# Kernel optimization log

Hardware: AMD Instinct MI355X
Metric: run time of the kernel (lower is better)

## Reference

```python
import jax, jax.numpy as jnp
import numpy as np

N = 50000      # nodes
E = 800000     # edges
F_IN = 11      # node feature dim (from docstring)
HID = 128      # hidden_channels
NC = 16        # num_classes
G = 64         # number of graphs in the batch
NEG_SLOPE = 0.2


def gat_layer(h_in, src, dst, W, a_src, a_dst, b, n_nodes):
    """Single-head GATConv with self-loops (PyG defaults, edge_attr unused)."""
    h = h_in @ W                                   # [N, C]
    alpha_s = h @ a_src                            # [N]
    alpha_d = h @ a_dst                            # [N]
    e = jax.nn.leaky_relu(alpha_s[src] + alpha_d[dst], NEG_SLOPE)  # [E']
    # segment softmax over incoming edges of each dst node
    m = jax.ops.segment_max(e, dst, num_segments=n_nodes)
    ex = jnp.exp(e - m[dst])
    den = jax.ops.segment_sum(ex, dst, num_segments=n_nodes)
    alpha = ex / den[dst]                          # [E']
    out = jax.ops.segment_sum(alpha[:, None] * h[src], dst, num_segments=n_nodes)
    return out + b


def setup_inputs() -> dict:
    key = jax.random.key(0)
    ks = jax.random.split(key, 16)
    glorot = lambda k, fi, fo: jax.random.normal(k, (fi, fo), jnp.float32) * np.float32(1.0 / np.sqrt(fi))
    inp = {
        "x": jax.random.normal(ks[0], (N, F_IN), jnp.float32),
        "edge_index": jax.random.randint(ks[1], (2, E), 0, N, dtype=jnp.int32),
        "edge_attr": jax.random.normal(ks[2], (E, 17), jnp.float32),
        "batch": jnp.sort(jax.random.randint(ks[3], (N,), 0, G, dtype=jnp.int32)),
        "W1": glorot(ks[4], F_IN, HID), "as1": jax.random.normal(ks[5], (HID,)) * 0.1,
        "ad1": jax.random.normal(ks[6], (HID,)) * 0.1, "b1": jnp.zeros((HID,), jnp.float32),
        "W2": glorot(ks[7], HID, HID), "as2": jax.random.normal(ks[8], (HID,)) * 0.1,
        "ad2": jax.random.normal(ks[9], (HID,)) * 0.1, "b2": jnp.zeros((HID,), jnp.float32),
        "W3": glorot(ks[10], HID, NC), "as3": jax.random.normal(ks[11], (NC,)) * 0.1,
        "ad3": jax.random.normal(ks[12], (NC,)) * 0.1, "b3": jnp.zeros((NC,), jnp.float32),
    }
    return inp


def reference(x, edge_index, edge_attr, batch,
              W1, as1, ad1, b1, W2, as2, ad2, b2, W3, as3, ad3, b3):
    n = x.shape[0]
    loop = jnp.arange(n, dtype=edge_index.dtype)
    src = jnp.concatenate([edge_index[0], loop])   # add self-loops
    dst = jnp.concatenate([edge_index[1], loop])

    h = jax.nn.relu(gat_layer(x, src, dst, W1, as1, ad1, b1, n))
    h = jax.nn.relu(gat_layer(h, src, dst, W2, as2, ad2, b2, n))
    h = jax.nn.relu(gat_layer(h, src, dst, W3, as3, ad3, b3, n))

    # global mean pool over graphs
    sums = jax.ops.segment_sum(h, batch, num_segments=G)              # [G, NC]
    cnts = jax.ops.segment_sum(jnp.ones((n,), h.dtype), batch, num_segments=G)
    pooled = sums / jnp.maximum(cnts, 1.0)[:, None]
    # dropout is identity in eval mode
    return jax.nn.sigmoid(pooled)
```

## Files before the change

kernel.cpp:

```cpp
#include <hip/hip_runtime.h>
#include <hip/hip_bf16.h>
#include <hip/hip_fp16.h>
#include <math.h>

#define N_NODES 50000
#define N_EDGES 800000
#define F_IN    11
#define HID     128
#define NC      16
#define NG      64
#define E_TOT   (N_EDGES + N_NODES)
#define NBLK_POOL ((N_NODES + 255) / 256)
#define NEG_SLOPE 0.2f

#define NB   ((N_NODES + 63) >> 6)
#define BCAP 4096
#define NHB  ((N_EDGES + 4095) / 4096)

typedef _Float16 half_t;
typedef __attribute__((ext_vector_type(2))) _Float16 half2v;
typedef __attribute__((ext_vector_type(4))) _Float16 half4;
typedef __attribute__((ext_vector_type(8))) _Float16 half8;
typedef __attribute__((ext_vector_type(4))) float f32x4;

__device__ __forceinline__ float leaky(float x) { return x >= 0.f ? x : NEG_SLOPE * x; }


__global__ __launch_bounds__(256) void bucket_hist_w2t_kernel(const int* __restrict__ ei,
                                                              int* __restrict__ gcount,
                                                              const float* __restrict__ W2,
                                                              half_t* __restrict__ W2T) {
    int tid = threadIdx.x;
    if (blockIdx.x >= NHB) {
        int id = (blockIdx.x - NHB) * 256 + tid;
        if (id < HID * HID) {
            int col = id >> 7, k = id & 127;
            W2T[id] = (half_t)W2[k * HID + col];
        }
        return;
    }
    __shared__ int cnt[NB];
    for (int i = tid; i < NB; i += 256) cnt[i] = 0;
    __syncthreads();
    int e0 = blockIdx.x * 4096 + tid;
#pragma unroll
    for (int k = 0; k < 16; ++k) {
        int e = e0 + k * 256;
        if (e < N_EDGES) atomicAdd(&cnt[ei[N_EDGES + e] >> 6], 1);
    }
    __syncthreads();
    for (int i = tid; i < NB; i += 256)
        if (cnt[i]) atomicAdd(&gcount[i], cnt[i]);
}

__global__ void scanB_kernel(const int* __restrict__ gcount, int* __restrict__ bOff,
                             int* __restrict__ gcur) {
    __shared__ int ls[1024];
    int tid = threadIdx.x;
    int v = 0;
    if (tid < NB) {
        int sl = N_NODES - (tid << 6);
        sl = sl > 64 ? 64 : sl;
        v = gcount[tid] + sl;
    }
    ls[tid] = v;
    __syncthreads();
    for (int ofs = 1; ofs < 1024; ofs <<= 1) {
        int x = (tid >= ofs) ? ls[tid - ofs] : 0;
        __syncthreads();
        ls[tid] += x;
        __syncthreads();
    }
    int excl = (tid > 0) ? ls[tid - 1] : 0;
    if (tid < NB) { bOff[tid] = excl; gcur[tid] = excl; }
    if (tid == 0) bOff[NB] = E_TOT;
}

__global__ __launch_bounds__(256) void bucket_scatter_kernel(const int* __restrict__ ei,
                                                             int* __restrict__ gcur,
                                                             unsigned* __restrict__ pairs) {
    __shared__ int cnt[NB];
    __shared__ int base[NB];
    int tid = threadIdx.x;
    for (int i = tid; i < NB; i += 256) cnt[i] = 0;
    __syncthreads();
    int s[16], d[16];
    int e0 = blockIdx.x * 4096 + tid;
#pragma unroll
    for (int k = 0; k < 16; ++k) {
        int e = e0 + k * 256;
        if (e < N_EDGES) { s[k] = ei[e]; d[k] = ei[N_EDGES + e]; }
        else if (e < E_TOT) { s[k] = d[k] = e - N_EDGES; }
        else d[k] = -1;
        if (d[k] >= 0) atomicAdd(&cnt[d[k] >> 6], 1);
    }
    __syncthreads();
    for (int i = tid; i < NB; i += 256)
        base[i] = cnt[i] ? atomicAdd(&gcur[i], cnt[i]) : 0;
    __syncthreads();
    for (int i = tid; i < NB; i += 256) cnt[i] = 0;
    __syncthreads();
#pragma unroll
    for (int k = 0; k < 16; ++k) {
        if (d[k] >= 0) {
            int b = d[k] >> 6;
            int r = atomicAdd(&cnt[b], 1);
            pairs[base[b] + r] = (unsigned)s[k] | ((unsigned)(d[k] & 63) << 16);
        }
    }
}

__global__ __launch_bounds__(256) void csr_finalize_kernel(const unsigned* __restrict__ pairs,
                                                           const int* __restrict__ bOff,
                                                           int* __restrict__ off,
                                                           int* __restrict__ csr) {
    __shared__ unsigned lp[BCAP];
    __shared__ int deg[64], offs[65], cnt[64];
    int b = blockIdx.x, tid = threadIdx.x;
    int d0 = b << 6;
    int nd = N_NODES - d0; nd = nd > 64 ? 64 : nd;
    int lo = bOff[b], hi = bOff[b + 1], n = hi - lo;
    if (tid < 64) { deg[tid] = 0; cnt[tid] = 0; }
    __syncthreads();
    bool staged = (n <= BCAP);
    for (int i = tid; i < n; i += 256) {
        unsigned p = pairs[lo + i];
        if (staged) lp[i] = p;
        atomicAdd(&deg[p >> 16], 1);
    }
    __syncthreads();
    if (tid == 0) {
        int a = 0;
#pragma unroll
        for (int i = 0; i < 64; ++i) { offs[i] = a; a += deg[i]; }
        offs[64] = a;
    }
    __syncthreads();
    if (tid < nd) off[d0 + tid] = lo + offs[tid];
    if (b == (int)gridDim.x - 1 && tid == 0) off[N_NODES] = E_TOT;
    for (int i = tid; i < n; i += 256) {
        unsigned p = staged ? lp[i] : pairs[lo + i];
        int ld = p >> 16;
        int r = atomicAdd(&cnt[ld], 1);
        csr[lo + offs[ld] + r] = (int)(p & 0xFFFF);
    }
}


__global__ void gemm1_kernel(const float* __restrict__ x, const float* __restrict__ W,
                             const float* __restrict__ a_s, const float* __restrict__ a_d,
                             half_t* __restrict__ h16,
                             float* __restrict__ asv, float* __restrict__ adv) {
    __shared__ float xr[F_IN];
    __shared__ float red[4];
    int row = blockIdx.x;
    int t = threadIdx.x;
    if (t < F_IN) xr[t] = x[row * F_IN + t];
    __syncthreads();
    float acc = 0.f;
#pragma unroll
    for (int k = 0; k < F_IN; ++k) acc = fmaf(xr[k], W[k * HID + t], acc);
    h16[(size_t)row * HID + t] = (half_t)acc;
    float ps = acc * a_s[t], pd = acc * a_d[t];
#pragma unroll
    for (int m = 32; m; m >>= 1) { ps += __shfl_xor(ps, m); pd += __shfl_xor(pd, m); }
    int lane = t & 63, wid = t >> 6;
    if (lane == 0) { red[wid * 2] = ps; red[wid * 2 + 1] = pd; }
    __syncthreads();
    if (t == 0) { asv[row] = red[0] + red[2]; adv[row] = red[1] + red[3]; }
}


__global__ __launch_bounds__(256) void gemm2_mfma_kernel(
    const half_t* __restrict__ A, const half_t* __restrict__ W2T,
    const float* __restrict__ a_s, const float* __restrict__ a_d,
    half_t* __restrict__ outp, float* __restrict__ asv, float* __restrict__ adv) {
    int wid = threadIdx.x >> 6;
    int lane = threadIdx.x & 63;
    int row0 = blockIdx.x * 64 + wid * 16;
    int rl = lane & 15;
    int kg = lane >> 4;
    int arow = row0 + rl;
    if (arow >= N_NODES) arow = N_NODES - 1;
    const half8* Ap = (const half8*)(A + (size_t)arow * HID);
    half8 afrag[4];
#pragma unroll
    for (int kk = 0; kk < 4; ++kk) afrag[kk] = Ap[kk * 4 + kg];
    float ps[4] = {0.f, 0.f, 0.f, 0.f}, pd[4] = {0.f, 0.f, 0.f, 0.f};
#pragma unroll
    for (int ct = 0; ct < 8; ++ct) {
        f32x4 acc = {0.f, 0.f, 0.f, 0.f};
        const half8* Bp = (const half8*)(W2T + (size_t)(ct * 16 + rl) * HID);
#pragma unroll
        for (int kk = 0; kk < 4; ++kk)
            acc = __builtin_amdgcn_mfma_f32_16x16x32_f16(afrag[kk], Bp[kk * 4 + kg], acc, 0, 0, 0);
        int col = ct * 16 + rl;
        float as_c = a_s[col], ad_c = a_d[col];
#pragma unroll
        for (int i = 0; i < 4; ++i) {
            int r = row0 + kg * 4 + i;
            ps[i] = fmaf(acc[i], as_c, ps[i]);
            pd[i] = fmaf(acc[i], ad_c, pd[i]);
            if (r < N_NODES) outp[(size_t)r * HID + col] = (half_t)acc[i];
        }
    }
#pragma unroll
    for (int m = 1; m <= 8; m <<= 1) {
#pragma unroll
        for (int i = 0; i < 4; ++i) { ps[i] += __shfl_xor(ps[i], m); pd[i] += __shfl_xor(pd[i], m); }
    }
    if (rl == 0) {
#pragma unroll
        for (int i = 0; i < 4; ++i) {
            int r = row0 + kg * 4 + i;
            if (r < N_NODES) { asv[r] = ps[i]; adv[r] = pd[i]; }
        }
    }
}


__global__ __launch_bounds__(256) void gemm3_kernel(const half_t* __restrict__ A16,
                                                    const float* __restrict__ W,
                                                    const float* __restrict__ a_s,
                                                    const float* __restrict__ a_d,
                                                    half_t* __restrict__ outp,
                                                    float* __restrict__ asv,
                                                    float* __restrict__ adv) {
    __shared__ float hs[16][HID + 1];
    int tid = threadIdx.x;
    int row0 = blockIdx.x * 16;
    for (int i = tid; i < 16 * HID; i += 256) {
        int r = i >> 7, c = i & 127;
        int gr = row0 + r;
        hs[r][c] = (gr < N_NODES) ? (float)A16[(size_t)gr * HID + c] : 0.f;
    }
    __syncthreads();
    int col = tid & 15, r = tid >> 4;
    float acc = 0.f;
#pragma unroll 4
    for (int k = 0; k < HID; ++k) acc = fmaf(hs[r][k], W[k * NC + col], acc);
    int gr = row0 + r;
    float ps = acc * a_s[col], pd = acc * a_d[col];
#pragma unroll
    for (int m = 1; m <= 8; m <<= 1) { ps += __shfl_xor(ps, m); pd += __shfl_xor(pd, m); }
    if (gr < N_NODES) {
        outp[(size_t)gr * NC + col] = (half_t)acc;
        if (col == 0) { asv[gr] = ps; adv[gr] = pd; }
    }
}


__global__ __launch_bounds__(256) void agg128_kernel(
    const half_t* __restrict__ h16, const int* __restrict__ off, const int* __restrict__ csr,
    const float* __restrict__ asv, const float* __restrict__ adv,
    const float* __restrict__ bias, half_t* __restrict__ outp) {
    int lane = threadIdx.x & 63;
    int n = (blockIdx.x * blockDim.x + threadIdx.x) >> 6;
    if (n >= N_NODES) return;
    int o0 = off[n], o1 = off[n + 1];
    float ad_n = adv[n];
    int half = lane >> 5;
    int qc = lane & 31;
    const half4* hp = (const half4*)h16;
    float m = -INFINITY, den = 0.f;
    float4 acc = make_float4(0.f, 0.f, 0.f, 0.f);
    for (int base = o0; base < o1; base += 64) {
        int j = base + lane;
        bool valid = j < o1;
        int s = valid ? csr[j] : 0;
        float e = valid ? leaky(asv[s] + ad_n) : -INFINITY;
        float cm = e;
#pragma unroll
        for (int k = 32; k; k >>= 1) cm = fmaxf(cm, __shfl_xor(cm, k));
        float nm = fmaxf(m, cm);
        float rs = __expf(m - nm);
        den *= rs; acc.x *= rs; acc.y *= rs; acc.z *= rs; acc.w *= rs;
        float w = valid ? __expf(e - nm) : 0.f;
        float ws = w;
#pragma unroll
        for (int k = 32; k; k >>= 1) ws += __shfl_xor(ws, k);
        den += ws;
        m = nm;
        int cnt = min(64, o1 - base);
        int t = 0;
        for (; t + 16 <= cnt; t += 16) {
            int sv[8]; float wv[8]; half4 vv[8];
#pragma unroll
            for (int u = 0; u < 8; ++u) {
                sv[u] = __shfl(s, t + 2 * u + half);
                wv[u] = __shfl(w, t + 2 * u + half);
            }
#pragma unroll
            for (int u = 0; u < 8; ++u) vv[u] = hp[(size_t)sv[u] * 32 + qc];
#pragma unroll
            for (int u = 0; u < 8; ++u) {
                acc.x = fmaf(wv[u], (float)vv[u].x, acc.x);
                acc.y = fmaf(wv[u], (float)vv[u].y, acc.y);
                acc.z = fmaf(wv[u], (float)vv[u].z, acc.z);
                acc.w = fmaf(wv[u], (float)vv[u].w, acc.w);
            }
        }
        for (; t + 8 <= cnt; t += 8) {
            int sv[4]; float wv[4]; half4 vv[4];
#pragma unroll
            for (int u = 0; u < 4; ++u) {
                sv[u] = __shfl(s, t + 2 * u + half);
                wv[u] = __shfl(w, t + 2 * u + half);
            }
#pragma unroll
            for (int u = 0; u < 4; ++u) vv[u] = hp[(size_t)sv[u] * 32 + qc];
#pragma unroll
            for (int u = 0; u < 4; ++u) {
                acc.x = fmaf(wv[u], (float)vv[u].x, acc.x);
                acc.y = fmaf(wv[u], (float)vv[u].y, acc.y);
                acc.z = fmaf(wv[u], (float)vv[u].z, acc.z);
                acc.w = fmaf(wv[u], (float)vv[u].w, acc.w);
            }
        }
        for (; t + 2 <= cnt; t += 2) {
            int s0 = __shfl(s, t + half);
            float w0 = __shfl(w, t + half);
            half4 v0 = hp[(size_t)s0 * 32 + qc];
            acc.x = fmaf(w0, (float)v0.x, acc.x); acc.y = fmaf(w0, (float)v0.y, acc.y);
            acc.z = fmaf(w0, (float)v0.z, acc.z); acc.w = fmaf(w0, (float)v0.w, acc.w);
        }
        if (t < cnt) {
            int s0 = __shfl(s, t);
            float w0 = __shfl(w, t);
            if (half == 0) {
                half4 v0 = hp[(size_t)s0 * 32 + qc];
                acc.x = fmaf(w0, (float)v0.x, acc.x); acc.y = fmaf(w0, (float)v0.y, acc.y);
                acc.z = fmaf(w0, (float)v0.z, acc.z); acc.w = fmaf(w0, (float)v0.w, acc.w);
            }
        }
    }
    acc.x += __shfl_xor(acc.x, 32); acc.y += __shfl_xor(acc.y, 32);
    acc.z += __shfl_xor(acc.z, 32); acc.w += __shfl_xor(acc.w, 32);
    if (half == 0) {
        float inv = 1.f / den;
        float4 bv = ((const float4*)bias)[qc];
        half4 o;
        o.x = (half_t)fmaxf(fmaf(acc.x, inv, bv.x), 0.f);
        o.y = (half_t)fmaxf(fmaf(acc.y, inv, bv.y), 0.f);
        o.z = (half_t)fmaxf(fmaf(acc.z, inv, bv.z), 0.f);
        o.w = (half_t)fmaxf(fmaf(acc.w, inv, bv.w), 0.f);
        ((half4*)outp)[(size_t)n * 32 + qc] = o;
    }
}

__global__ __launch_bounds__(256) void agg16_kernel(
    const half_t* __restrict__ h, const int* __restrict__ off, const int* __restrict__ csr,
    const float* __restrict__ asv, const float* __restrict__ adv,
    const float* __restrict__ bias, float* __restrict__ outp) {
    int lane = threadIdx.x & 63;
    int n = (blockIdx.x * blockDim.x + threadIdx.x) >> 6;
    if (n >= N_NODES) return;
    int o0 = off[n], o1 = off[n + 1];
    float ad_n = adv[n];
    int g = lane >> 3, pr = lane & 7;
    const half2v* hp = (const half2v*)h;
    float m = -INFINITY, den = 0.f;
    float ax = 0.f, ay = 0.f;
    for (int base = o0; base < o1; base += 64) {
        int j = base + lane;
        bool valid = j < o1;
        int s = valid ? csr[j] : 0;
        float e = valid ? leaky(asv[s] + ad_n) : -INFINITY;
        float cm = e;
#pragma unroll
        for (int k = 32; k; k >>= 1) cm = fmaxf(cm, __shfl_xor(cm, k));
        float nm = fmaxf(m, cm);
        float rs = __expf(m - nm);
        den *= rs; ax *= rs; ay *= rs;
        float w = valid ? __expf(e - nm) : 0.f;
        float ws = w;
#pragma unroll
        for (int k = 32; k; k >>= 1) ws += __shfl_xor(ws, k);
        den += ws;
        m = nm;
        int cnt = min(64, o1 - base);
        for (int t = g; t < cnt; t += 8) {
            int st = __shfl(s, t);
            float wt = __shfl(w, t);
            half2v v = hp[(size_t)st * 8 + pr];
            ax = fmaf(wt, (float)v.x, ax); ay = fmaf(wt, (float)v.y, ay);
        }
    }
    ax += __shfl_xor(ax, 8);  ay += __shfl_xor(ay, 8);
    ax += __shfl_xor(ax, 16); ay += __shfl_xor(ay, 16);
    ax += __shfl_xor(ax, 32); ay += __shfl_xor(ay, 32);
    if (g == 0) {
        float inv = 1.f / den;
        float vx = fmaxf(fmaf(ax, inv, bias[pr * 2]), 0.f);
        float vy = fmaxf(fmaf(ay, inv, bias[pr * 2 + 1]), 0.f);
        ((float2*)outp)[(size_t)n * 8 + pr] = make_float2(vx, vy);
    }
}


__global__ void pool_partial_kernel(const float* __restrict__ h3, const int* __restrict__ batch,
                                    float* __restrict__ part) {
    __shared__ float sp[NG * 17];
    int tid = threadIdx.x;
    for (int i = tid; i < NG * 17; i += 256) sp[i] = 0.f;
    __syncthreads();
    int n = blockIdx.x * 256 + tid;
    if (n < N_NODES) {
        int g = batch[n];
        const float4* hv = (const float4*)(h3 + (size_t)n * NC);
#pragma unroll
        for (int j = 0; j < 4; ++j) {
            float4 v = hv[j];
            atomicAdd(&sp[g * 17 + j * 4 + 0], v.x);
            atomicAdd(&sp[g * 17 + j * 4 + 1], v.y);
            atomicAdd(&sp[g * 17 + j * 4 + 2], v.z);
            atomicAdd(&sp[g * 17 + j * 4 + 3], v.w);
        }
        atomicAdd(&sp[g * 17 + 16], 1.f);
    }
    __syncthreads();
    for (int i = tid; i < NG * 17; i += 256) part[(size_t)blockIdx.x * (NG * 17) + i] = sp[i];
}

__global__ void pool_final_kernel(const float* __restrict__ part, float* __restrict__ outp) {
    int tid = threadIdx.x;
    int g = tid >> 4, c = tid & 15;
    float sum = 0.f, cnt = 0.f;
    for (int b = 0; b < NBLK_POOL; ++b) {
        sum += part[(size_t)b * (NG * 17) + g * 17 + c];
        cnt += part[(size_t)b * (NG * 17) + g * 17 + 16];
    }
    float v = sum / fmaxf(cnt, 1.f);
    outp[g * NC + c] = 1.f / (1.f + __expf(-v));
}


extern "C" void kernel_launch(void* const* d_in, const int* in_sizes, int n_in,
                              void* d_out, int out_size, void* d_ws, size_t ws_size,
                              hipStream_t stream) {
    const float* x   = (const float*)d_in[0];
    const int*   ei  = (const int*)d_in[1];
    const int*   bat = (const int*)d_in[3];
    const float* W1  = (const float*)d_in[4];
    const float* as1 = (const float*)d_in[5];
    const float* ad1 = (const float*)d_in[6];
    const float* b1  = (const float*)d_in[7];
    const float* W2  = (const float*)d_in[8];
    const float* as2 = (const float*)d_in[9];
    const float* ad2 = (const float*)d_in[10];
    const float* b2  = (const float*)d_in[11];
    const float* W3  = (const float*)d_in[12];
    const float* as3 = (const float*)d_in[13];
    const float* ad3 = (const float*)d_in[14];
    const float* b3  = (const float*)d_in[15];
    float* outp = (float*)d_out;

    char* p = (char*)d_ws;
    auto carve = [&](size_t bytes) {
        char* r = p;
        p += (bytes + 255) & ~(size_t)255;
        return r;
    };
    int*      off    = (int*)carve((size_t)(N_NODES + 1) * 4);
    int*      csr    = (int*)carve((size_t)E_TOT * 4);
    int*      gcount = (int*)carve((size_t)NB * 4);
    int*      bOff   = (int*)carve((size_t)(NB + 1) * 4);
    int*      gcur   = (int*)carve((size_t)NB * 4);
    unsigned* pairs  = (unsigned*)carve((size_t)E_TOT * 4);
    half_t*   h16    = (half_t*)carve((size_t)N_NODES * HID * 2);
    half_t*   o16    = (half_t*)carve((size_t)N_NODES * HID * 2);
    half_t*   W2T    = (half_t*)carve((size_t)HID * HID * 2);
    half_t*   h3     = (half_t*)carve((size_t)N_NODES * NC * 2);
    float*    o3     = (float*)carve((size_t)N_NODES * NC * 4);
    float*    asv    = (float*)carve((size_t)N_NODES * 4);
    float*    adv    = (float*)carve((size_t)N_NODES * 4);
    float*    part   = (float*)carve((size_t)NBLK_POOL * NG * 17 * 4);

    hipMemsetAsync(gcount, 0, (size_t)NB * 4, stream);
    bucket_hist_w2t_kernel<<<NHB + 64, 256, 0, stream>>>(ei, gcount, W2, W2T);
    scanB_kernel<<<1, 1024, 0, stream>>>(gcount, bOff, gcur);
    bucket_scatter_kernel<<<(E_TOT + 4095) / 4096, 256, 0, stream>>>(ei, gcur, pairs);
    csr_finalize_kernel<<<NB, 256, 0, stream>>>(pairs, bOff, off, csr);

    gemm1_kernel<<<N_NODES, 128, 0, stream>>>(x, W1, as1, ad1, h16, asv, adv);
    agg128_kernel<<<(N_NODES + 3) / 4, 256, 0, stream>>>(h16, off, csr, asv, adv, b1, o16);

    gemm2_mfma_kernel<<<(N_NODES + 63) / 64, 256, 0, stream>>>(o16, W2T, as2, ad2, h16, asv, adv);
    agg128_kernel<<<(N_NODES + 3) / 4, 256, 0, stream>>>(h16, off, csr, asv, adv, b2, o16);

    gemm3_kernel<<<(N_NODES + 15) / 16, 256, 0, stream>>>(o16, W3, as3, ad3, h3, asv, adv);
    agg16_kernel<<<(N_NODES + 3) / 4, 256, 0, stream>>>(h3, off, csr, asv, adv, b3, o3);

    pool_partial_kernel<<<NBLK_POOL, 256, 0, stream>>>(o3, bat, part);
    pool_final_kernel<<<1, 1024, 0, stream>>>(part, outp);
}
```

Before: 340.7 us.

## Fuse all GAT stages into one persistent cooperative kernel with grid syncs

Replaces the sequence of about twelve kernel launches (CSR build, three GEMM+aggregate layers, pooling) with a single cooperative persistent kernel. The stages are separated by grid.sync and use grid-stride loops over waves, and a shared-memory union serves the different phases. The aim is to remove launch gaps and tail effects between the many small kernels. The cost is that grid-wide barriers and a fixed occupancy-limited grid size may reduce parallelism in the memory-bound aggregation phases. A multi-kernel fallback is kept in case the cooperative launch fails.

```diff
diff --git a/kernel.cpp b/kernel.cpp
--- a/kernel.cpp
+++ b/kernel.cpp
@@ -1,7 +1,10 @@
 #include <hip/hip_runtime.h>
+#include <hip/hip_cooperative_groups.h>
 #include <hip/hip_bf16.h>
 #include <hip/hip_fp16.h>
 #include <math.h>
+
+namespace cg = cooperative_groups;
 
 #define N_NODES 50000
 #define N_EDGES 800000
@@ -16,6 +19,7 @@
 #define NB   ((N_NODES + 63) >> 6)
 #define BCAP 4096
 #define NHB  ((N_EDGES + 4095) / 4096)
+#define NSC  ((E_TOT + 4095) / 4096)
 
 typedef _Float16 half_t;
 typedef __attribute__((ext_vector_type(2))) _Float16 half2v;
@@ -26,10 +30,469 @@
 __device__ __forceinline__ float leaky(float x) { return x >= 0.f ? x : NEG_SLOPE * x; }
 
 
-__global__ __launch_bounds__(256) void bucket_hist_w2t_kernel(const int* __restrict__ ei,
-                                                              int* __restrict__ gcount,
-                                                              const float* __restrict__ W2,
-                                                              half_t* __restrict__ W2T) {
+__device__ __forceinline__ void gemm1_body(const float* __restrict__ x,
+                                           const float* __restrict__ W1,
+                                           const float* __restrict__ a_s,
+                                           const float* __restrict__ a_d,
+                                           half_t* __restrict__ h16,
+                                           float* __restrict__ asv, float* __restrict__ adv,
+                                           int gwave, int nwaves, int lane) {
+    int c0 = lane * 2, c1 = lane * 2 + 1;
+    for (int row = gwave; row < N_NODES; row += nwaves) {
+        const float* xr = x + (size_t)row * F_IN;
+        float a0 = 0.f, a1 = 0.f;
+#pragma unroll
+        for (int k = 0; k < F_IN; ++k) {
+            float xv = xr[k];
+            a0 = fmaf(xv, W1[k * HID + c0], a0);
+            a1 = fmaf(xv, W1[k * HID + c1], a1);
+        }
+        half2v hv; hv.x = (half_t)a0; hv.y = (half_t)a1;
+        ((half2v*)(h16 + (size_t)row * HID))[lane] = hv;
+        float ps = a0 * a_s[c0] + a1 * a_s[c1];
+        float pd = a0 * a_d[c0] + a1 * a_d[c1];
+#pragma unroll
+        for (int m = 32; m; m >>= 1) { ps += __shfl_xor(ps, m); pd += __shfl_xor(pd, m); }
+        if (lane == 0) { asv[row] = ps; adv[row] = pd; }
+    }
+}
+
+__device__ __forceinline__ void gemm2_body(const half_t* __restrict__ A,
+                                           const half_t* __restrict__ W2T,
+                                           const float* __restrict__ a_s,
+                                           const float* __restrict__ a_d,
+                                           half_t* __restrict__ outp,
+                                           float* __restrict__ asv, float* __restrict__ adv,
+                                           int gwave, int nwaves, int lane) {
+    int rl = lane & 15, kg = lane >> 4;
+    for (int row0 = gwave * 16; row0 < N_NODES; row0 += nwaves * 16) {
+        int arow = row0 + rl;
+        if (arow >= N_NODES) arow = N_NODES - 1;
+        const half8* Ap = (const half8*)(A + (size_t)arow * HID);
+        half8 afrag[4];
+#pragma unroll
+        for (int kk = 0; kk < 4; ++kk) afrag[kk] = Ap[kk * 4 + kg];
+        float ps[4] = {0.f, 0.f, 0.f, 0.f}, pd[4] = {0.f, 0.f, 0.f, 0.f};
+#pragma unroll
+        for (int ct = 0; ct < 8; ++ct) {
+            f32x4 acc = {0.f, 0.f, 0.f, 0.f};
+            const half8* Bp = (const half8*)(W2T + (size_t)(ct * 16 + rl) * HID);
+#pragma unroll
+            for (int kk = 0; kk < 4; ++kk)
+                acc = __builtin_amdgcn_mfma_f32_16x16x32_f16(afrag[kk], Bp[kk * 4 + kg], acc, 0, 0, 0);
+            int col = ct * 16 + rl;
+            float as_c = a_s[col], ad_c = a_d[col];
+#pragma unroll
+            for (int i = 0; i < 4; ++i) {
+                int r = row0 + kg * 4 + i;
+                ps[i] = fmaf(acc[i], as_c, ps[i]);
+                pd[i] = fmaf(acc[i], ad_c, pd[i]);
+                if (r < N_NODES) outp[(size_t)r * HID + col] = (half_t)acc[i];
+            }
+        }
+#pragma unroll
+        for (int m = 1; m <= 8; m <<= 1) {
+#pragma unroll
+            for (int i = 0; i < 4; ++i) { ps[i] += __shfl_xor(ps[i], m); pd[i] += __shfl_xor(pd[i], m); }
+        }
+        if (rl == 0) {
+#pragma unroll
+            for (int i = 0; i < 4; ++i) {
+                int r = row0 + kg * 4 + i;
+                if (r < N_NODES) { asv[r] = ps[i]; adv[r] = pd[i]; }
+            }
+        }
+    }
+}
+
+__device__ __forceinline__ void agg128_body(const half_t* __restrict__ h16,
+                                            const int* __restrict__ off,
+                                            const int* __restrict__ csr,
+                                            const float* __restrict__ asv,
+                                            const float* __restrict__ adv,
+                                            const float* __restrict__ bias,
+                                            half_t* __restrict__ outp,
+                                            int gwave, int nwaves, int lane) {
+    int hw = lane >> 5;
+    int qc = lane & 31;
+    const half4* hp = (const half4*)h16;
+    for (int n = gwave; n < N_NODES; n += nwaves) {
+        int o0 = off[n], o1 = off[n + 1];
+        float ad_n = adv[n];
+        float m = -INFINITY, den = 0.f;
+        float4 acc = make_float4(0.f, 0.f, 0.f, 0.f);
+        for (int base = o0; base < o1; base += 64) {
+            int j = base + lane;
+            bool valid = j < o1;
+            int s = valid ? csr[j] : 0;
+            float e = valid ? leaky(asv[s] + ad_n) : -INFINITY;
+            float cm = e;
+#pragma unroll
+            for (int k = 32; k; k >>= 1) cm = fmaxf(cm, __shfl_xor(cm, k));
+            float nm = fmaxf(m, cm);
+            float rs = __expf(m - nm);
+            den *= rs; acc.x *= rs; acc.y *= rs; acc.z *= rs; acc.w *= rs;
+            float w = valid ? __expf(e - nm) : 0.f;
+            float ws = w;
+#pragma unroll
+            for (int k = 32; k; k >>= 1) ws += __shfl_xor(ws, k);
+            den += ws;
+            m = nm;
+            int cnt = min(64, o1 - base);
+            int t = 0;
+            for (; t + 16 <= cnt; t += 16) {
+                int sv[8]; float wv[8]; half4 vv[8];
+#pragma unroll
+                for (int u = 0; u < 8; ++u) {
+                    sv[u] = __shfl(s, t + 2 * u + hw);
+                    wv[u] = __shfl(w, t + 2 * u + hw);
+                }
+#pragma unroll
+                for (int u = 0; u < 8; ++u) vv[u] = hp[(size_t)sv[u] * 32 + qc];
+#pragma unroll
+                for (int u = 0; u < 8; ++u) {
+                    acc.x = fmaf(wv[u], (float)vv[u].x, acc.x);
+                    acc.y = fmaf(wv[u], (float)vv[u].y, acc.y);
+                    acc.z = fmaf(wv[u], (float)vv[u].z, acc.z);
+                    acc.w = fmaf(wv[u], (float)vv[u].w, acc.w);
+                }
+            }
+            for (; t + 8 <= cnt; t += 8) {
+                int sv[4]; float wv[4]; half4 vv[4];
+#pragma unroll
+                for (int u = 0; u < 4; ++u) {
+                    sv[u] = __shfl(s, t + 2 * u + hw);
+                    wv[u] = __shfl(w, t + 2 * u + hw);
+                }
+#pragma unroll
+                for (int u = 0; u < 4; ++u) vv[u] = hp[(size_t)sv[u] * 32 + qc];
+#pragma unroll
+                for (int u = 0; u < 4; ++u) {
+                    acc.x = fmaf(wv[u], (float)vv[u].x, acc.x);
+                    acc.y = fmaf(wv[u], (float)vv[u].y, acc.y);
+                    acc.z = fmaf(wv[u], (float)vv[u].z, acc.z);
+                    acc.w = fmaf(wv[u], (float)vv[u].w, acc.w);
+                }
+            }
+            for (; t + 2 <= cnt; t += 2) {
+                int s0 = __shfl(s, t + hw);
+                float w0 = __shfl(w, t + hw);
+                half4 v0 = hp[(size_t)s0 * 32 + qc];
+                acc.x = fmaf(w0, (float)v0.x, acc.x); acc.y = fmaf(w0, (float)v0.y, acc.y);
+                acc.z = fmaf(w0, (float)v0.z, acc.z); acc.w = fmaf(w0, (float)v0.w, acc.w);
+            }
+            if (t < cnt) {
+                int s0 = __shfl(s, t);
+                float w0 = __shfl(w, t);
+                if (hw == 0) {
+                    half4 v0 = hp[(size_t)s0 * 32 + qc];
+                    acc.x = fmaf(w0, (float)v0.x, acc.x); acc.y = fmaf(w0, (float)v0.y, acc.y);
+                    acc.z = fmaf(w0, (float)v0.z, acc.z); acc.w = fmaf(w0, (float)v0.w, acc.w);
+                }
+            }
+        }
+        acc.x += __shfl_xor(acc.x, 32); acc.y += __shfl_xor(acc.y, 32);
+        acc.z += __shfl_xor(acc.z, 32); acc.w += __shfl_xor(acc.w, 32);
+        if (hw == 0) {
+            float inv = 1.f / den;
+            float4 bv = ((const float4*)bias)[qc];
+            half4 o;
+            o.x = (half_t)fmaxf(fmaf(acc.x, inv, bv.x), 0.f);
+            o.y = (half_t)fmaxf(fmaf(acc.y, inv, bv.y), 0.f);
+            o.z = (half_t)fmaxf(fmaf(acc.z, inv, bv.z), 0.f);
+            o.w = (half_t)fmaxf(fmaf(acc.w, inv, bv.w), 0.f);
+            ((half4*)outp)[(size_t)n * 32 + qc] = o;
+        }
+    }
+}
+
+__device__ __forceinline__ void agg16_body(const half_t* __restrict__ h,
+                                           const int* __restrict__ off,
+                                           const int* __restrict__ csr,
+                                           const float* __restrict__ asv,
+                                           const float* __restrict__ adv,
+                                           const float* __restrict__ bias,
+                                           float* __restrict__ outp,
+                                           int gwave, int nwaves, int lane) {
+    int g = lane >> 3, pr = lane & 7;
+    const half2v* hp = (const half2v*)h;
+    for (int n = gwave; n < N_NODES; n += nwaves) {
+        int o0 = off[n], o1 = off[n + 1];
+        float ad_n = adv[n];
+        float m = -INFINITY, den = 0.f;
+        float ax = 0.f, ay = 0.f;
+        for (int base = o0; base < o1; base += 64) {
+            int j = base + lane;
+            bool valid = j < o1;
+            int s = valid ? csr[j] : 0;
+            float e = valid ? leaky(asv[s] + ad_n) : -INFINITY;
+            float cm = e;
+#pragma unroll
+            for (int k = 32; k; k >>= 1) cm = fmaxf(cm, __shfl_xor(cm, k));
+            float nm = fmaxf(m, cm);
+            float rs = __expf(m - nm);
+            den *= rs; ax *= rs; ay *= rs;
+            float w = valid ? __expf(e - nm) : 0.f;
+            float ws = w;
+#pragma unroll
+            for (int k = 32; k; k >>= 1) ws += __shfl_xor(ws, k);
+            den += ws;
+            m = nm;
+            int cnt = min(64, o1 - base);
+            for (int t = g; t < cnt; t += 8) {
+                int st = __shfl(s, t);
+                float wt = __shfl(w, t);
+                half2v v = hp[(size_t)st * 8 + pr];
+                ax = fmaf(wt, (float)v.x, ax); ay = fmaf(wt, (float)v.y, ay);
+            }
+        }
+        ax += __shfl_xor(ax, 8);  ay += __shfl_xor(ay, 8);
+        ax += __shfl_xor(ax, 16); ay += __shfl_xor(ay, 16);
+        ax += __shfl_xor(ax, 32); ay += __shfl_xor(ay, 32);
+        if (g == 0) {
+            float inv = 1.f / den;
+            float vx = fmaxf(fmaf(ax, inv, bias[pr * 2]), 0.f);
+            float vy = fmaxf(fmaf(ay, inv, bias[pr * 2 + 1]), 0.f);
+            ((float2*)outp)[(size_t)n * 8 + pr] = make_float2(vx, vy);
+        }
+    }
+}
+
+__device__ __forceinline__ void pool_final_body(const float* __restrict__ part,
+                                                float* __restrict__ outp,
+                                                int gid, int gstride) {
+    for (int o = gid; o < NG * NC; o += gstride) {
+        int g = o >> 4, c = o & 15;
+        float sum = 0.f, cntv = 0.f;
+        for (int b = 0; b < NBLK_POOL; ++b) {
+            sum  += part[(size_t)b * (NG * 17) + g * 17 + c];
+            cntv += part[(size_t)b * (NG * 17) + g * 17 + 16];
+        }
+        float v = sum / fmaxf(cntv, 1.f);
+        outp[o] = 1.f / (1.f + __expf(-v));
+    }
+}
+
+
+struct MegaArgs {
+    const float* x; const int* ei; const int* bat;
+    const float* W1; const float* as1; const float* ad1; const float* b1;
+    const float* W2; const float* as2; const float* ad2; const float* b2;
+    const float* W3; const float* as3; const float* ad3; const float* b3;
+    float* outp;
+    int* off; int* csr; int* gcount; int* bOff; int* gcur; unsigned* pairs;
+    half_t* h16; half_t* o16; half_t* W2T; half_t* h3; float* o3;
+    float* asv; float* adv; float* part;
+};
+
+union SharedU {
+    int hist_cnt[NB];
+    struct { int cnt[NB]; int base[NB]; } scat;
+    struct { unsigned lp[BCAP]; int deg[64]; int offs[65]; int cnt[64]; } fin;
+    int scan_ls[256];
+    float hs[16][HID + 1];
+    float sp[NG * 17];
+};
+
+__global__ __launch_bounds__(256, 4) void gat_mega_kernel(MegaArgs P) {
+    cg::grid_group grid = cg::this_grid();
+    const int tid = threadIdx.x;
+    const int bid = blockIdx.x;
+    const int G = gridDim.x;
+    const int gthread = bid * 256 + tid;
+    const int nthreads = G * 256;
+    const int wid = tid >> 6, lane = tid & 63;
+    const int gwave = bid * 4 + wid, nwaves = G * 4;
+    __shared__ SharedU u;
+
+    for (int i = gthread; i < NB; i += nthreads) P.gcount[i] = 0;
+    grid.sync();
+
+    for (int c = bid; c < NHB + 64; c += G) {
+        if (c < NHB) {
+            for (int i = tid; i < NB; i += 256) u.hist_cnt[i] = 0;
+            __syncthreads();
+            int e0 = c * 4096 + tid;
+#pragma unroll
+            for (int k = 0; k < 16; ++k) {
+                int e = e0 + k * 256;
+                if (e < N_EDGES) atomicAdd(&u.hist_cnt[P.ei[N_EDGES + e] >> 6], 1);
+            }
+            __syncthreads();
+            for (int i = tid; i < NB; i += 256)
+                if (u.hist_cnt[i]) atomicAdd(&P.gcount[i], u.hist_cnt[i]);
+            __syncthreads();
+        } else {
+            int id = (c - NHB) * 256 + tid;
+            if (id < HID * HID) {
+                int col = id >> 7, k = id & 127;
+                P.W2T[id] = (half_t)P.W2[k * HID + col];
+            }
+        }
+    }
+    grid.sync();
+
+    if (bid == 0) {
+        int base = tid * 4;
+        int v0 = 0, v1 = 0, v2 = 0, v3 = 0;
+        if (base + 0 < NB) v0 = P.gcount[base + 0] + min(64, N_NODES - ((base + 0) << 6));
+        if (base + 1 < NB) v1 = P.gcount[base + 1] + min(64, N_NODES - ((base + 1) << 6));
+        if (base + 2 < NB) v2 = P.gcount[base + 2] + min(64, N_NODES - ((base + 2) << 6));
+        if (base + 3 < NB) v3 = P.gcount[base + 3] + min(64, N_NODES - ((base + 3) << 6));
+        int pre1 = v0, pre2 = v0 + v1, pre3 = v0 + v1 + v2;
+        u.scan_ls[tid] = pre3 + v3;
+        __syncthreads();
+        for (int ofs = 1; ofs < 256; ofs <<= 1) {
+            int xv = (tid >= ofs) ? u.scan_ls[tid - ofs] : 0;
+            __syncthreads();
+            u.scan_ls[tid] += xv;
+            __syncthreads();
+        }
+        int excl = (tid > 0) ? u.scan_ls[tid - 1] : 0;
+        if (base + 0 < NB) { P.bOff[base + 0] = excl;        P.gcur[base + 0] = excl; }
+        if (base + 1 < NB) { P.bOff[base + 1] = excl + pre1; P.gcur[base + 1] = excl + pre1; }
+        if (base + 2 < NB) { P.bOff[base + 2] = excl + pre2; P.gcur[base + 2] = excl + pre2; }
+        if (base + 3 < NB) { P.bOff[base + 3] = excl + pre3; P.gcur[base + 3] = excl + pre3; }
+        if (tid == 0) P.bOff[NB] = E_TOT;
+    }
+    grid.sync();
+
+    for (int c = bid; c < NSC; c += G) {
+        for (int i = tid; i < NB; i += 256) u.scat.cnt[i] = 0;
+        __syncthreads();
+        int s[16], d[16];
+        int e0 = c * 4096 + tid;
+#pragma unroll
+        for (int k = 0; k < 16; ++k) {
+            int e = e0 + k * 256;
+            if (e < N_EDGES) { s[k] = P.ei[e]; d[k] = P.ei[N_EDGES + e]; }
+            else if (e < E_TOT) { s[k] = d[k] = e - N_EDGES; }
+            else d[k] = -1;
+            if (d[k] >= 0) atomicAdd(&u.scat.cnt[d[k] >> 6], 1);
+        }
+        __syncthreads();
+        for (int i = tid; i < NB; i += 256)
+            u.scat.base[i] = u.scat.cnt[i] ? atomicAdd(&P.gcur[i], u.scat.cnt[i]) : 0;
+        __syncthreads();
+        for (int i = tid; i < NB; i += 256) u.scat.cnt[i] = 0;
+        __syncthreads();
+#pragma unroll
+        for (int k = 0; k < 16; ++k) {
+            if (d[k] >= 0) {
+                int b = d[k] >> 6;
+                int r = atomicAdd(&u.scat.cnt[b], 1);
+                P.pairs[u.scat.base[b] + r] = (unsigned)s[k] | ((unsigned)(d[k] & 63) << 16);
+            }
+        }
+        __syncthreads();
+    }
+    grid.sync();
+
+    if (bid == 0 && tid == 0) P.off[N_NODES] = E_TOT;
+    for (int b = bid; b < NB; b += G) {
+        int d0 = b << 6;
+        int nd = N_NODES - d0; nd = nd > 64 ? 64 : nd;
+        int lo = P.bOff[b], hi = P.bOff[b + 1], n = hi - lo;
+        if (tid < 64) { u.fin.deg[tid] = 0; u.fin.cnt[tid] = 0; }
+        __syncthreads();
+        bool staged = (n <= BCAP);
+        for (int i = tid; i < n; i += 256) {
+            unsigned pp = P.pairs[lo + i];
+            if (staged) u.fin.lp[i] = pp;
+            atomicAdd(&u.fin.deg[pp >> 16], 1);
+        }
+        __syncthreads();
+        if (tid == 0) {
+            int a = 0;
+#pragma unroll
+            for (int i = 0; i < 64; ++i) { u.fin.offs[i] = a; a += u.fin.deg[i]; }
+            u.fin.offs[64] = a;
+        }
+        __syncthreads();
+        if (tid < nd) P.off[d0 + tid] = lo + u.fin.offs[tid];
+        for (int i = tid; i < n; i += 256) {
+            unsigned pp = staged ? u.fin.lp[i] : P.pairs[lo + i];
+            int ld = pp >> 16;
+            int r = atomicAdd(&u.fin.cnt[ld], 1);
+            P.csr[lo + u.fin.offs[ld] + r] = (int)(pp & 0xFFFF);
+        }
+        __syncthreads();
+    }
+    grid.sync();
+
+    gemm1_body(P.x, P.W1, P.as1, P.ad1, P.h16, P.asv, P.adv, gwave, nwaves, lane);
+    grid.sync();
+
+    agg128_body(P.h16, P.off, P.csr, P.asv, P.adv, P.b1, P.o16, gwave, nwaves, lane);
+    grid.sync();
+
+    gemm2_body(P.o16, P.W2T, P.as2, P.ad2, P.h16, P.asv, P.adv, gwave, nwaves, lane);
+    grid.sync();
+
+    agg128_body(P.h16, P.off, P.csr, P.asv, P.adv, P.b2, P.o16, gwave, nwaves, lane);
+    grid.sync();
+
+    {
+        const int NG3 = (N_NODES + 15) / 16;
+        int col = tid & 15, r = tid >> 4;
+        for (int blk = bid; blk < NG3; blk += G) {
+            int row0 = blk * 16;
+            for (int i = tid; i < 16 * HID; i += 256) {
+                int rr = i >> 7, cc = i & 127;
+                int gr = row0 + rr;
+                u.hs[rr][cc] = (gr < N_NODES) ? (float)P.o16[(size_t)gr * HID + cc] : 0.f;
+            }
+            __syncthreads();
+            float acc = 0.f;
+#pragma unroll 4
+            for (int k = 0; k < HID; ++k) acc = fmaf(u.hs[r][k], P.W3[k * NC + col], acc);
+            int gr = row0 + r;
+            float ps = acc * P.as3[col], pd = acc * P.ad3[col];
+#pragma unroll
+            for (int m = 1; m <= 8; m <<= 1) { ps += __shfl_xor(ps, m); pd += __shfl_xor(pd, m); }
+            if (gr < N_NODES) {
+                P.h3[(size_t)gr * NC + col] = (half_t)acc;
+                if (col == 0) { P.asv[gr] = ps; P.adv[gr] = pd; }
+            }
+            __syncthreads();
+        }
+    }
+    grid.sync();
+
+    agg16_body(P.h3, P.off, P.csr, P.asv, P.adv, P.b3, P.o3, gwave, nwaves, lane);
+    grid.sync();
+
+    for (int blk = bid; blk < NBLK_POOL; blk += G) {
+        for (int i = tid; i < NG * 17; i += 256) u.sp[i] = 0.f;
+        __syncthreads();
+        int n = blk * 256 + tid;
+        if (n < N_NODES) {
+            int g = P.bat[n];
+            const float4* hv = (const float4*)(P.o3 + (size_t)n * NC);
+#pragma unroll
+            for (int j = 0; j < 4; ++j) {
+                float4 v = hv[j];
+                atomicAdd(&u.sp[g * 17 + j * 4 + 0], v.x);
+                atomicAdd(&u.sp[g * 17 + j * 4 + 1], v.y);
+                atomicAdd(&u.sp[g * 17 + j * 4 + 2], v.z);
+                atomicAdd(&u.sp[g * 17 + j * 4 + 3], v.w);
+            }
+            atomicAdd(&u.sp[g * 17 + 16], 1.f);
+        }
+        __syncthreads();
+        for (int i = tid; i < NG * 17; i += 256) P.part[(size_t)blk * (NG * 17) + i] = u.sp[i];
+        __syncthreads();
+    }
+    grid.sync();
+
+    pool_final_body(P.part, P.outp, gthread, nthreads);
+}
+
+
+__global__ __launch_bounds__(256) void fb_hist_w2t_kernel(const int* __restrict__ ei,
+                                                          int* __restrict__ gcount,
+                                                          const float* __restrict__ W2,
+                                                          half_t* __restrict__ W2T) {
     int tid = threadIdx.x;
     if (blockIdx.x >= NHB) {
         int id = (blockIdx.x - NHB) * 256 + tid;
@@ -53,8 +516,8 @@
         if (cnt[i]) atomicAdd(&gcount[i], cnt[i]);
 }
 
-__global__ void scanB_kernel(const int* __restrict__ gcount, int* __restrict__ bOff,
-                             int* __restrict__ gcur) {
+__global__ void fb_scanB_kernel(const int* __restrict__ gcount, int* __restrict__ bOff,
+                                int* __restrict__ gcur) {
     __shared__ int ls[1024];
     int tid = threadIdx.x;
     int v = 0;
@@ -76,9 +539,9 @@
     if (tid == 0) bOff[NB] = E_TOT;
 }
 
-__global__ __launch_bounds__(256) void bucket_scatter_kernel(const int* __restrict__ ei,
-                                                             int* __restrict__ gcur,
-                                                             unsigned* __restrict__ pairs) {
+__global__ __launch_bounds__(256) void fb_scatter_kernel(const int* __restrict__ ei,
+                                                         int* __restrict__ gcur,
+                                                         unsigned* __restrict__ pairs) {
     __shared__ int cnt[NB];
     __shared__ int base[NB];
     int tid = threadIdx.x;
@@ -110,10 +573,10 @@
     }
 }
 
-__global__ __launch_bounds__(256) void csr_finalize_kernel(const unsigned* __restrict__ pairs,
-                                                           const int* __restrict__ bOff,
-                                                           int* __restrict__ off,
-                                                           int* __restrict__ csr) {
+__global__ __launch_bounds__(256) void fb_finalize_kernel(const unsigned* __restrict__ pairs,
+                                                          const int* __restrict__ bOff,
+                                                          int* __restrict__ off,
+                                                          int* __restrict__ csr) {
     __shared__ unsigned lp[BCAP];
     __shared__ int deg[64], offs[65], cnt[64];
     int b = blockIdx.x, tid = threadIdx.x;
@@ -146,86 +609,27 @@
     }
 }
 
-
-__global__ void gemm1_kernel(const float* __restrict__ x, const float* __restrict__ W,
-                             const float* __restrict__ a_s, const float* __restrict__ a_d,
-                             half_t* __restrict__ h16,
-                             float* __restrict__ asv, float* __restrict__ adv) {
-    __shared__ float xr[F_IN];
-    __shared__ float red[4];
-    int row = blockIdx.x;
-    int t = threadIdx.x;
-    if (t < F_IN) xr[t] = x[row * F_IN + t];
-    __syncthreads();
-    float acc = 0.f;
-#pragma unroll
-    for (int k = 0; k < F_IN; ++k) acc = fmaf(xr[k], W[k * HID + t], acc);
-    h16[(size_t)row * HID + t] = (half_t)acc;
-    float ps = acc * a_s[t], pd = acc * a_d[t];
-#pragma unroll
-    for (int m = 32; m; m >>= 1) { ps += __shfl_xor(ps, m); pd += __shfl_xor(pd, m); }
-    int lane = t & 63, wid = t >> 6;
-    if (lane == 0) { red[wid * 2] = ps; red[wid * 2 + 1] = pd; }
-    __syncthreads();
-    if (t == 0) { asv[row] = red[0] + red[2]; adv[row] = red[1] + red[3]; }
-}
-
-
-__global__ __launch_bounds__(256) void gemm2_mfma_kernel(
-    const half_t* __restrict__ A, const half_t* __restrict__ W2T,
-    const float* __restrict__ a_s, const float* __restrict__ a_d,
-    half_t* __restrict__ outp, float* __restrict__ asv, float* __restrict__ adv) {
-    int wid = threadIdx.x >> 6;
+__global__ __launch_bounds__(256) void fb_gemm1_kernel(const float* x, const float* W1,
+                                                       const float* a_s, const float* a_d,
+                                                       half_t* h16, float* asv, float* adv) {
     int lane = threadIdx.x & 63;
-    int row0 = blockIdx.x * 64 + wid * 16;
-    int rl = lane & 15;
-    int kg = lane >> 4;
-    int arow = row0 + rl;
-    if (arow >= N_NODES) arow = N_NODES - 1;
-    const half8* Ap = (const half8*)(A + (size_t)arow * HID);
-    half8 afrag[4];
-#pragma unroll
-    for (int kk = 0; kk < 4; ++kk) afrag[kk] = Ap[kk * 4 + kg];
-    float ps[4] = {0.f, 0.f, 0.f, 0.f}, pd[4] = {0.f, 0.f, 0.f, 0.f};
-#pragma unroll
-    for (int ct = 0; ct < 8; ++ct) {
-        f32x4 acc = {0.f, 0.f, 0.f, 0.f};
-        const half8* Bp = (const half8*)(W2T + (size_t)(ct * 16 + rl) * HID);
-#pragma unroll
-        for (int kk = 0; kk < 4; ++kk)
-            acc = __builtin_amdgcn_mfma_f32_16x16x32_f16(afrag[kk], Bp[kk * 4 + kg], acc, 0, 0, 0);
-        int col = ct * 16 + rl;
-        float as_c = a_s[col], ad_c = a_d[col];
-#pragma unroll
-        for (int i = 0; i < 4; ++i) {
-            int r = row0 + kg * 4 + i;
-            ps[i] = fmaf(acc[i], as_c, ps[i]);
-            pd[i] = fmaf(acc[i], ad_c, pd[i]);
-            if (r < N_NODES) outp[(size_t)r * HID + col] = (half_t)acc[i];
-        }
-    }
-#pragma unroll
-    for (int m = 1; m <= 8; m <<= 1) {
-#pragma unroll
-        for (int i = 0; i < 4; ++i) { ps[i] += __shfl_xor(ps[i], m); pd[i] += __shfl_xor(pd[i], m); }
-    }
-    if (rl == 0) {
-#pragma unroll
-        for (int i = 0; i < 4; ++i) {
-            int r = row0 + kg * 4 + i;
-            if (r < N_NODES) { asv[r] = ps[i]; adv[r] = pd[i]; }
-        }
-    }
-}
-
-
-__global__ __launch_bounds__(256) void gemm3_kernel(const half_t* __restrict__ A16,
-                                                    const float* __restrict__ W,
-                                                    const float* __restrict__ a_s,
-                                                    const float* __restrict__ a_d,
-                                                    half_t* __restrict__ outp,
-                                                    float* __restrict__ asv,
-                                                    float* __restrict__ adv) {
+    int gwave = (blockIdx.x * blockDim.x + threadIdx.x) >> 6;
+    int nwaves = (gridDim.x * blockDim.x) >> 6;
+    gemm1_body(x, W1, a_s, a_d, h16, asv, adv, gwave, nwaves, lane);
+}
+
+__global__ __launch_bounds__(256) void fb_gemm2_kernel(const half_t* A, const half_t* W2T,
+                                                       const float* a_s, const float* a_d,
+                                                       half_t* outp, float* asv, float* adv) {
+    int lane = threadIdx.x & 63;
+    int gwave = (blockIdx.x * blockDim.x + threadIdx.x) >> 6;
+    int nwaves = (gridDim.x * blockDim.x) >> 6;
+    gemm2_body(A, W2T, a_s, a_d, outp, asv, adv, gwave, nwaves, lane);
+}
+
+__global__ __launch_bounds__(256) void fb_gemm3_kernel(const half_t* A16, const float* W,
+                                                       const float* a_s, const float* a_d,
+                                                       half_t* outp, float* asv, float* adv) {
     __shared__ float hs[16][HID + 1];
     int tid = threadIdx.x;
     int row0 = blockIdx.x * 16;
@@ -249,157 +653,28 @@
     }
 }
 
-
-__global__ __launch_bounds__(256) void agg128_kernel(
-    const half_t* __restrict__ h16, const int* __restrict__ off, const int* __restrict__ csr,
-    const float* __restrict__ asv, const float* __restrict__ adv,
-    const float* __restrict__ bias, half_t* __restrict__ outp) {
+__global__ __launch_bounds__(256) void fb_agg128_kernel(const half_t* h16, const int* off,
+                                                        const int* csr, const float* asv,
+                                                        const float* adv, const float* bias,
+                                                        half_t* outp) {
     int lane = threadIdx.x & 63;
-    int n = (blockIdx.x * blockDim.x + threadIdx.x) >> 6;
-    if (n >= N_NODES) return;
-    int o0 = off[n], o1 = off[n + 1];
-    float ad_n = adv[n];
-    int half = lane >> 5;
-    int qc = lane & 31;
-    const half4* hp = (const half4*)h16;
-    float m = -INFINITY, den = 0.f;
-    float4 acc = make_float4(0.f, 0.f, 0.f, 0.f);
-    for (int base = o0; base < o1; base += 64) {
-        int j = base + lane;
-        bool valid = j < o1;
-        int s = valid ? csr[j] : 0;
-        float e = valid ? leaky(asv[s] + ad_n) : -INFINITY;
-        float cm = e;
-#pragma unroll
-        for (int k = 32; k; k >>= 1) cm = fmaxf(cm, __shfl_xor(cm, k));
-        float nm = fmaxf(m, cm);
-        float rs = __expf(m - nm);
-        den *= rs; acc.x *= rs; acc.y *= rs; acc.z *= rs; acc.w *= rs;
-        float w = valid ? __expf(e - nm) : 0.f;
-        float ws = w;
-#pragma unroll
-        for (int k = 32; k; k >>= 1) ws += __shfl_xor(ws, k);
-        den += ws;
-        m = nm;
-        int cnt = min(64, o1 - base);
-        int t = 0;
-        for (; t + 16 <= cnt; t += 16) {
-            int sv[8]; float wv[8]; half4 vv[8];
-#pragma unroll
-            for (int u = 0; u < 8; ++u) {
-                sv[u] = __shfl(s, t + 2 * u + half);
-                wv[u] = __shfl(w, t + 2 * u + half);
-            }
-#pragma unroll
-            for (int u = 0; u < 8; ++u) vv[u] = hp[(size_t)sv[u] * 32 + qc];
-#pragma unroll
-            for (int u = 0; u < 8; ++u) {
-                acc.x = fmaf(wv[u], (float)vv[u].x, acc.x);
-                acc.y = fmaf(wv[u], (float)vv[u].y, acc.y);
-                acc.z = fmaf(wv[u], (float)vv[u].z, acc.z);
-                acc.w = fmaf(wv[u], (float)vv[u].w, acc.w);
-            }
-        }
-        for (; t + 8 <= cnt; t += 8) {
-            int sv[4]; float wv[4]; half4 vv[4];
-#pragma unroll
-            for (int u = 0; u < 4; ++u) {
-                sv[u] = __shfl(s, t + 2 * u + half);
-                wv[u] = __shfl(w, t + 2 * u + half);
-            }
-#pragma unroll
-            for (int u = 0; u < 4; ++u) vv[u] = hp[(size_t)sv[u] * 32 + qc];
-#pragma unroll
-            for (int u = 0; u < 4; ++u) {
-                acc.x = fmaf(wv[u], (float)vv[u].x, acc.x);
-                acc.y = fmaf(wv[u], (float)vv[u].y, acc.y);
-                acc.z = fmaf(wv[u], (float)vv[u].z, acc.z);
-                acc.w = fmaf(wv[u], (float)vv[u].w, acc.w);
-            }
-        }
-        for (; t + 2 <= cnt; t += 2) {
-            int s0 = __shfl(s, t + half);
-            float w0 = __shfl(w, t + half);
-            half4 v0 = hp[(size_t)s0 * 32 + qc];
-            acc.x = fmaf(w0, (float)v0.x, acc.x); acc.y = fmaf(w0, (float)v0.y, acc.y);
-            acc.z = fmaf(w0, (float)v0.z, acc.z); acc.w = fmaf(w0, (float)v0.w, acc.w);
-        }
-        if (t < cnt) {
-            int s0 = __shfl(s, t);
-            float w0 = __shfl(w, t);
-            if (half == 0) {
-                half4 v0 = hp[(size_t)s0 * 32 + qc];
-                acc.x = fmaf(w0, (float)v0.x, acc.x); acc.y = fmaf(w0, (float)v0.y, acc.y);
-                acc.z = fmaf(w0, (float)v0.z, acc.z); acc.w = fmaf(w0, (float)v0.w, acc.w);
-            }
-        }
-    }
-    acc.x += __shfl_xor(acc.x, 32); acc.y += __shfl_xor(acc.y, 32);
-    acc.z += __shfl_xor(acc.z, 32); acc.w += __shfl_xor(acc.w, 32);
-    if (half == 0) {
-        float inv = 1.f / den;
-        float4 bv = ((const float4*)bias)[qc];
-        half4 o;
-        o.x = (half_t)fmaxf(fmaf(acc.x, inv, bv.x), 0.f);
-        o.y = (half_t)fmaxf(fmaf(acc.y, inv, bv.y), 0.f);
-        o.z = (half_t)fmaxf(fmaf(acc.z, inv, bv.z), 0.f);
-        o.w = (half_t)fmaxf(fmaf(acc.w, inv, bv.w), 0.f);
-        ((half4*)outp)[(size_t)n * 32 + qc] = o;
-    }
-}
-
-__global__ __launch_bounds__(256) void agg16_kernel(
-    const half_t* __restrict__ h, const int* __restrict__ off, const int* __restrict__ csr,
-    const float* __restrict__ asv, const float* __restrict__ adv,
-    const float* __restrict__ bias, float* __restrict__ outp) {
+    int gwave = (blockIdx.x * blockDim.x + threadIdx.x) >> 6;
+    int nwaves = (gridDim.x * blockDim.x) >> 6;
+    agg128_body(h16, off, csr, asv, adv, bias, outp, gwave, nwaves, lane);
+}
+
+__global__ __launch_bounds__(256) void fb_agg16_kernel(const half_t* h, const int* off,
+                                                       const int* csr, const float* asv,
+                                                       const float* adv, const float* bias,
+                                                       float* outp) {
     int lane = threadIdx.x & 63;
-    int n = (blockIdx.x * blockDim.x + threadIdx.x) >> 6;
-    if (n >= N_NODES) return;
-    int o0 = off[n], o1 = off[n + 1];
-    float ad_n = adv[n];
-    int g = lane >> 3, pr = lane & 7;
-    const half2v* hp = (const half2v*)h;
-    float m = -INFINITY, den = 0.f;
-    float ax = 0.f, ay = 0.f;
-    for (int base = o0; base < o1; base += 64) {
-        int j = base + lane;
-        bool valid = j < o1;
-        int s = valid ? csr[j] : 0;
-        float e = valid ? leaky(asv[s] + ad_n) : -INFINITY;
-        float cm = e;
-#pragma unroll
-        for (int k = 32; k; k >>= 1) cm = fmaxf(cm, __shfl_xor(cm, k));
-        float nm = fmaxf(m, cm);
-        float rs = __expf(m - nm);
-        den *= rs; ax *= rs; ay *= rs;
-        float w = valid ? __expf(e - nm) : 0.f;
-        float ws = w;
-#pragma unroll
-        for (int k = 32; k; k >>= 1) ws += __shfl_xor(ws, k);
-        den += ws;
-        m = nm;
-        int cnt = min(64, o1 - base);
-        for (int t = g; t < cnt; t += 8) {
-            int st = __shfl(s, t);
-            float wt = __shfl(w, t);
-            half2v v = hp[(size_t)st * 8 + pr];
-            ax = fmaf(wt, (float)v.x, ax); ay = fmaf(wt, (float)v.y, ay);
-        }
-    }
-    ax += __shfl_xor(ax, 8);  ay += __shfl_xor(ay, 8);
-    ax += __shfl_xor(ax, 16); ay += __shfl_xor(ay, 16);
-    ax += __shfl_xor(ax, 32); ay += __shfl_xor(ay, 32);
-    if (g == 0) {
-        float inv = 1.f / den;
-        float vx = fmaxf(fmaf(ax, inv, bias[pr * 2]), 0.f);
-        float vy = fmaxf(fmaf(ay, inv, bias[pr * 2 + 1]), 0.f);
-        ((float2*)outp)[(size_t)n * 8 + pr] = make_float2(vx, vy);
-    }
-}
-
-
-__global__ void pool_partial_kernel(const float* __restrict__ h3, const int* __restrict__ batch,
-                                    float* __restrict__ part) {
+    int gwave = (blockIdx.x * blockDim.x + threadIdx.x) >> 6;
+    int nwaves = (gridDim.x * blockDim.x) >> 6;
+    agg16_body(h, off, csr, asv, adv, bias, outp, gwave, nwaves, lane);
+}
+
+__global__ void fb_pool_partial_kernel(const float* __restrict__ h3, const int* __restrict__ batch,
+                                       float* __restrict__ part) {
     __shared__ float sp[NG * 17];
     int tid = threadIdx.x;
     for (int i = tid; i < NG * 17; i += 256) sp[i] = 0.f;
@@ -422,16 +697,8 @@
     for (int i = tid; i < NG * 17; i += 256) part[(size_t)blockIdx.x * (NG * 17) + i] = sp[i];
 }
 
-__global__ void pool_final_kernel(const float* __restrict__ part, float* __restrict__ outp) {
-    int tid = threadIdx.x;
-    int g = tid >> 4, c = tid & 15;
-    float sum = 0.f, cnt = 0.f;
-    for (int b = 0; b < NBLK_POOL; ++b) {
-        sum += part[(size_t)b * (NG * 17) + g * 17 + c];
-        cnt += part[(size_t)b * (NG * 17) + g * 17 + 16];
-    }
-    float v = sum / fmaxf(cnt, 1.f);
-    outp[g * NC + c] = 1.f / (1.f + __expf(-v));
+__global__ void fb_pool_final_kernel(const float* __restrict__ part, float* __restrict__ outp) {
+    pool_final_body(part, outp, blockIdx.x * 256 + threadIdx.x, gridDim.x * 256);
 }
 
 
@@ -476,21 +743,41 @@
     float*    adv    = (float*)carve((size_t)N_NODES * 4);
     float*    part   = (float*)carve((size_t)NBLK_POOL * NG * 17 * 4);
 
-    hipMemsetAsync(gcount, 0, (size_t)NB * 4, stream);
-    bucket_hist_w2t_kernel<<<NHB + 64, 256, 0, stream>>>(ei, gcount, W2, W2T);
-    scanB_kernel<<<1, 1024, 0, stream>>>(gcount, bOff, gcur);
-    bucket_scatter_kernel<<<(E_TOT + 4095) / 4096, 256, 0, stream>>>(ei, gcur, pairs);
-    csr_finalize_kernel<<<NB, 256, 0, stream>>>(pairs, bOff, off, csr);
-
-    gemm1_kernel<<<N_NODES, 128, 0, stream>>>(x, W1, as1, ad1, h16, asv, adv);
-    agg128_kernel<<<(N_NODES + 3) / 4, 256, 0, stream>>>(h16, off, csr, asv, adv, b1, o16);
-
-    gemm2_mfma_kernel<<<(N_NODES + 63) / 64, 256, 0, stream>>>(o16, W2T, as2, ad2, h16, asv, adv);
-    agg128_kernel<<<(N_NODES + 3) / 4, 256, 0, stream>>>(h16, off, csr, asv, adv, b2, o16);
-
-    gemm3_kernel<<<(N_NODES + 15) / 16, 256, 0, stream>>>(o16, W3, as3, ad3, h3, asv, adv);
-    agg16_kernel<<<(N_NODES + 3) / 4, 256, 0, stream>>>(h3, off, csr, asv, adv, b3, o3);
-
-    pool_partial_kernel<<<NBLK_POOL, 256, 0, stream>>>(o3, bat, part);
-    pool_final_kernel<<<1, 1024, 0, stream>>>(part, outp);
-}
+    MegaArgs prm;
+    prm.x = x; prm.ei = ei; prm.bat = bat;
+    prm.W1 = W1; prm.as1 = as1; prm.ad1 = ad1; prm.b1 = b1;
+    prm.W2 = W2; prm.as2 = as2; prm.ad2 = ad2; prm.b2 = b2;
+    prm.W3 = W3; prm.as3 = as3; prm.ad3 = ad3; prm.b3 = b3;
+    prm.outp = outp;
+    prm.off = off; prm.csr = csr; prm.gcount = gcount; prm.bOff = bOff;
+    prm.gcur = gcur; prm.pairs = pairs;
+    prm.h16 = h16; prm.o16 = o16; prm.W2T = W2T; prm.h3 = h3; prm.o3 = o3;
+    prm.asv = asv; prm.adv = adv; prm.part = part;
+
+    int perCU = 0;
+    hipError_t oe = hipOccupancyMaxActiveBlocksPerMultiprocessor(
+        &perCU, (const void*)gat_mega_kernel, 256, 0);
+    if (oe != hipSuccess || perCU < 1) { (void)hipGetLastError(); perCU = 2; }
+    int G = perCU * 256;
+    if (G > 2048) G = 2048;
+
+    void* args[] = { &prm };
+    hipError_t err = hipLaunchCooperativeKernel((const void*)gat_mega_kernel,
+                                                dim3(G), dim3(256), args, 0, stream);
+    if (err != hipSuccess) {
+        (void)hipGetLastError();
+        hipMemsetAsync(gcount, 0, (size_t)NB * 4, stream);
+        fb_hist_w2t_kernel<<<NHB + 64, 256, 0, stream>>>(ei, gcount, W2, W2T);
+        fb_scanB_kernel<<<1, 1024, 0, stream>>>(gcount, bOff, gcur);
+        fb_scatter_kernel<<<NSC, 256, 0, stream>>>(ei, gcur, pairs);
+        fb_finalize_kernel<<<NB, 256, 0, stream>>>(pairs, bOff, off, csr);
+        fb_gemm1_kernel<<<(N_NODES + 3) / 4, 256, 0, stream>>>(x, W1, as1, ad1, h16, asv, adv);
+        fb_agg128_kernel<<<(N_NODES + 3) / 4, 256, 0, stream>>>(h16, off, csr, asv, adv, b1, o16);
+        fb_gemm2_kernel<<<(N_NODES / 64 + 3) / 4, 256, 0, stream>>>(o16, W2T, as2, ad2, h16, asv, adv);
+        fb_agg128_kernel<<<(N_NODES + 3) / 4, 256, 0, stream>>>(h16, off, csr, asv, adv, b2, o16);
+        fb_gemm3_kernel<<<(N_NODES + 15) / 16, 256, 0, stream>>>(o16, W3, as3, ad3, h3, asv, adv);
+        fb_agg16_kernel<<<(N_NODES + 3) / 4, 256, 0, stream>>>(h3, off, csr, asv, adv, b3, o3);
+        fb_pool_partial_kernel<<<NBLK_POOL, 256, 0, stream>>>(o3, bat, part);
+        fb_pool_final_kernel<<<4, 256, 0, stream>>>(part, outp);
+    }
+}
```

Result: slower. 1.129 ms (+231.2%).
